# Kernel optimization log

Measured on AMD Instinct MI355X. Metric: run time of the kernel, lower is better.

The kernel has to match this reference:

```python
import jax, jax.numpy as jnp
import numpy as np


def setup_inputs() -> dict:
    key = jax.random.key(0)
    k1, k2 = jax.random.split(key)
    n = 8192
    predictions = jax.random.normal(k1, (n,), dtype=jnp.float32)
    true_labels = jax.random.normal(k2, (n,), dtype=jnp.float32)
    return {"predictions": predictions, "true_labels": true_labels}


def reference(predictions, true_labels):
    n = predictions.shape[0]
    # Pairwise sign products: S[i,j] = sign(p_i - p_j) * sign(t_i - t_j).
    # S is symmetric with zero diagonal, so sum over i<j == sum(S) / 2.
    sp = jnp.sign(predictions[:, None] - predictions[None, :])  # [n, n]
    st = jnp.sign(true_labels[:, None] - true_labels[None, :])  # [n, n]
    numerator = jnp.sum(sp * st) * 0.5
    loss = 1.0 - 2.0 * numerator / (n * (n - 1))
    return loss
```

## Files before the change

kernel.cpp:

```cpp
#include <hip/hip_runtime.h>


constexpr int TI = 256;
constexpr int TJ = 256;

__global__ __launch_bounds__(256) void ktau_pairs(
    const float* __restrict__ p, const float* __restrict__ t,
    int* __restrict__ total, int n) {
  __shared__ float sp[TJ];
  __shared__ float st[TJ];
  const int tid = threadIdx.x;
  const int i   = blockIdx.x * TI + tid;
  const int j0  = blockIdx.y * TJ;
  const int jmax = min(TJ, n - j0);

  if (tid < jmax) {
    sp[tid] = p[j0 + tid];
    st[tid] = t[j0 + tid];
  }
  float pi = 0.0f, ti = 0.0f;
  if (i < n) { pi = p[i]; ti = t[i]; }
  __syncthreads();

  int acc = 0;
  if (i < n) {
#pragma unroll 8
    for (int k = 0; k < jmax; ++k) {
      float d = (pi - sp[k]) * (ti - st[k]);
      acc += (d > 0.0f) - (d < 0.0f);
    }
  }

  for (int off = 32; off > 0; off >>= 1)
    acc += __shfl_down(acc, off, 64);

  __shared__ int wsum[4];
  if ((tid & 63) == 0) wsum[tid >> 6] = acc;
  __syncthreads();
  if (tid == 0)
    atomicAdd(total, wsum[0] + wsum[1] + wsum[2] + wsum[3]);
}

__global__ void ktau_final(const int* __restrict__ total,
                           float* __restrict__ out, int n) {
  long long denom = (long long)n * (long long)(n - 1);
  out[0] = 1.0f - (float)((double)(*total) / (double)denom);
}

extern "C" void kernel_launch(void* const* d_in, const int* in_sizes, int n_in,
                              void* d_out, int out_size, void* d_ws, size_t ws_size,
                              hipStream_t stream) {
  const float* p = (const float*)d_in[0];
  const float* t = (const float*)d_in[1];
  float* out = (float*)d_out;
  int* total = (int*)d_ws;
  const int n = in_sizes[0];

  hipMemsetAsync(total, 0, sizeof(int), stream);

  dim3 grid((n + TI - 1) / TI, (n + TJ - 1) / TJ);
  ktau_pairs<<<grid, TI, 0, stream>>>(p, t, total, n);
  ktau_final<<<1, 1, 0, stream>>>(total, out, n);
}
```

Before: 74.47 us.

## Count discordant pairs via comparisons, register-block rows, drop atomics for partials

The pair loop now counts discordant pairs with two float comparisons and an XOR in place of a subtract-multiply-sign sequence. Each thread handles four i values held in registers, so every shared-memory load of the interleaved (p,t) float2 is reused four times. Per-block atomics and the memset are replaced by a partial-sum buffer that a 256-thread final kernel reduces, and the loss is rebuilt as n(n-1) minus twice the discordant count. Ties, which never occur with continuous random inputs, are now counted differently from the sign-based reference.

```diff
diff --git a/kernel.cpp b/kernel.cpp
--- a/kernel.cpp
+++ b/kernel.cpp
@@ -1,50 +1,76 @@
 #include <hip/hip_runtime.h>
 
 
-constexpr int TI = 256;
-constexpr int TJ = 256;
+constexpr int BLK = 256;
+constexpr int IPT = 4;
+constexpr int TI  = BLK * IPT;
+constexpr int TJ  = 128;
 
-__global__ __launch_bounds__(256) void ktau_pairs(
+__global__ __launch_bounds__(BLK) void ktau_pairs(
     const float* __restrict__ p, const float* __restrict__ t,
-    int* __restrict__ total, int n) {
-  __shared__ float sp[TJ];
-  __shared__ float st[TJ];
+    int* __restrict__ partial, int n) {
+  __shared__ float2 jv[TJ];
   const int tid = threadIdx.x;
-  const int i   = blockIdx.x * TI + tid;
+  const int i0  = blockIdx.x * TI;
   const int j0  = blockIdx.y * TJ;
   const int jmax = min(TJ, n - j0);
 
-  if (tid < jmax) {
-    sp[tid] = p[j0 + tid];
-    st[tid] = t[j0 + tid];
+  if (tid < jmax) jv[tid] = make_float2(p[j0 + tid], t[j0 + tid]);
+
+  float pi[IPT], ti[IPT];
+#pragma unroll
+  for (int m = 0; m < IPT; ++m) {
+    int i = i0 + tid + m * BLK;
+    int ic = i < n ? i : 0;
+    pi[m] = p[ic];
+    ti[m] = t[ic];
   }
-  float pi = 0.0f, ti = 0.0f;
-  if (i < n) { pi = p[i]; ti = t[i]; }
   __syncthreads();
 
-  int acc = 0;
-  if (i < n) {
+  int acc[IPT] = {};
 #pragma unroll 8
-    for (int k = 0; k < jmax; ++k) {
-      float d = (pi - sp[k]) * (ti - st[k]);
-      acc += (d > 0.0f) - (d < 0.0f);
-    }
+  for (int k = 0; k < jmax; ++k) {
+    float2 v = jv[k];
+#pragma unroll
+    for (int m = 0; m < IPT; ++m)
+      acc[m] += (int)((pi[m] < v.x) != (ti[m] < v.y));
   }
 
+  int sum = 0;
+#pragma unroll
+  for (int m = 0; m < IPT; ++m)
+    sum += (i0 + tid + m * BLK < n) ? acc[m] : 0;
+
   for (int off = 32; off > 0; off >>= 1)
-    acc += __shfl_down(acc, off, 64);
-
-  __shared__ int wsum[4];
-  if ((tid & 63) == 0) wsum[tid >> 6] = acc;
+    sum += __shfl_down(sum, off, 64);
+  __shared__ int wsum[BLK / 64];
+  if ((tid & 63) == 0) wsum[tid >> 6] = sum;
   __syncthreads();
-  if (tid == 0)
-    atomicAdd(total, wsum[0] + wsum[1] + wsum[2] + wsum[3]);
+  if (tid == 0) {
+    int s = 0;
+#pragma unroll
+    for (int w = 0; w < BLK / 64; ++w) s += wsum[w];
+    partial[blockIdx.y * gridDim.x + blockIdx.x] = s;
+  }
 }
 
-__global__ void ktau_final(const int* __restrict__ total,
-                           float* __restrict__ out, int n) {
-  long long denom = (long long)n * (long long)(n - 1);
-  out[0] = 1.0f - (float)((double)(*total) / (double)denom);
+__global__ __launch_bounds__(256) void ktau_final(
+    const int* __restrict__ partial, int nparts,
+    float* __restrict__ out, int n) {
+  const int tid = threadIdx.x;
+  long long sum = 0;
+  for (int idx = tid; idx < nparts; idx += 256) sum += partial[idx];
+  for (int off = 32; off > 0; off >>= 1)
+    sum += __shfl_down(sum, off, 64);
+  __shared__ long long wsum[4];
+  if ((tid & 63) == 0) wsum[tid >> 6] = sum;
+  __syncthreads();
+  if (tid == 0) {
+    long long disc = wsum[0] + wsum[1] + wsum[2] + wsum[3];
+    double nn = (double)n * (double)(n - 1);
+    double S = nn - 2.0 * (double)disc;
+    out[0] = (float)(1.0 - S / nn);
+  }
 }
 
 extern "C" void kernel_launch(void* const* d_in, const int* in_sizes, int n_in,
@@ -53,12 +79,13 @@
   const float* p = (const float*)d_in[0];
   const float* t = (const float*)d_in[1];
   float* out = (float*)d_out;
-  int* total = (int*)d_ws;
+  int* partial = (int*)d_ws;
   const int n = in_sizes[0];
 
-  hipMemsetAsync(total, 0, sizeof(int), stream);
+  const int gx = (n + TI - 1) / TI;
+  const int gy = (n + TJ - 1) / TJ;
+  dim3 grid(gx, gy);
 
-  dim3 grid((n + TI - 1) / TI, (n + TJ - 1) / TJ);
-  ktau_pairs<<<grid, TI, 0, stream>>>(p, t, total, n);
-  ktau_final<<<1, 1, 0, stream>>>(total, out, n);
+  ktau_pairs<<<grid, BLK, 0, stream>>>(p, t, partial, n);
+  ktau_final<<<1, 256, 0, stream>>>(partial, gx * gy, out, n);
 }
```

Result: faster. 64.16 us (-13.8%).
